# Performance work log

Measured on AMD Instinct MI355X. Metric: run time of the kernel, lower is better.

The kernel has to match this reference:

```python
import jax, jax.numpy as jnp
import numpy as np
import math

N_EMBD = 768
N_HEAD = 12
HEAD_DIM = N_EMBD // N_HEAD


def rope_cache(T, dim):
    # (T, dim//2, 2) with cos/sin of pos * inv_freq
    inv_freq = 1.0 / (10000.0 ** (2.0 * jnp.arange(dim // 2, dtype=jnp.float32) / dim))
    angles = jnp.arange(T, dtype=jnp.float32)[:, None] * inv_freq[None, :]
    return jnp.stack((jnp.cos(angles), jnp.sin(angles)), axis=-1)


def apply_rope(x, rope):
    # x: (B, H, T, D); rope: (T, D//2, 2)
    B, H, T, D = x.shape
    xp = x.reshape(B, H, T, D // 2, 2)
    x1, x2 = xp[..., 0], xp[..., 1]
    cos = rope[None, None, :, :, 0]
    sin = rope[None, None, :, :, 1]
    out = jnp.stack((x1 * cos - x2 * sin, x1 * sin + x2 * cos), axis=-1)
    return out.reshape(B, H, T, D)


def setup_inputs() -> dict:
    key = jax.random.key(0)
    ks = jax.random.split(key, 9)
    s = 0.02
    d = N_EMBD
    return {
        "x": jax.random.normal(ks[0], (2, 4096, d), dtype=jnp.float32),
        "Wq": jax.random.normal(ks[1], (d, d), dtype=jnp.float32) * s,
        "bq": jnp.zeros((d,), jnp.float32),
        "Wk": jax.random.normal(ks[2], (d, d), dtype=jnp.float32) * s,
        "bk": jnp.zeros((d,), jnp.float32),
        "Wv": jax.random.normal(ks[3], (d, d), dtype=jnp.float32) * s,
        "bv": jnp.zeros((d,), jnp.float32),
        "Wp": jax.random.normal(ks[4], (d, d), dtype=jnp.float32) * s,
        "bp": jnp.zeros((d,), jnp.float32),
    }


def reference(x, Wq, bq, Wk, bk, Wv, bv, Wp, bp):
    B, T, C = x.shape
    H, D = N_HEAD, HEAD_DIM

    def heads(W, b):
        return (x @ W.T + b).reshape(B, T, H, D).transpose(0, 2, 1, 3)

    q = heads(Wq, bq)
    k = heads(Wk, bk)
    v = heads(Wv, bv)
    rope = rope_cache(T, D)
    q = apply_rope(q, rope)
    k = apply_rope(k, rope)

    att = jnp.einsum('bhqd,bhkd->bhqk', q, k) * (1.0 / math.sqrt(D))
    causal = jnp.tril(jnp.ones((T, T), dtype=bool))
    att = jnp.where(causal[None, None], att, -jnp.inf)
    att = jax.nn.softmax(att, axis=-1)
    y = jnp.einsum('bhqk,bhkd->bhqd', att, v)
    y = y.transpose(0, 2, 1, 3).reshape(B, T, C)
    return y @ Wp.T + bp
```

## Files before the change

kernel.cpp:

```cpp
#include <hip/hip_runtime.h>
#include <hip/hip_bf16.h>

#define B_  2
#define T_  4096
#define C_  768
#define H_  12
#define D_  64
#define BT_ (B_*T_)

typedef __attribute__((ext_vector_type(8))) short short8;
typedef __attribute__((ext_vector_type(4))) short short4b;
typedef __attribute__((ext_vector_type(4))) float f32x4;

union U32x2 { unsigned u[2]; short4b s4; };

__device__ __forceinline__ ushort f2bf(float f) {
  union { __hip_bfloat16 b; ushort u; } cv; cv.b = __float2bfloat16(f); return cv.u;
}
__device__ __forceinline__ float bf2f(ushort u) {
  unsigned x = ((unsigned)u) << 16; float f; __builtin_memcpy(&f, &x, 4); return f;
}
__device__ __forceinline__ unsigned pack2(float a, float b) {
  return (unsigned)f2bf(a) | ((unsigned)f2bf(b) << 16);
}

__device__ __forceinline__ void gl16(const ushort* g, ushort* l) {
  typedef const __attribute__((address_space(1))) unsigned GU;
  typedef __attribute__((address_space(3))) unsigned LU;
  __builtin_amdgcn_global_load_lds((GU*)g, (LU*)l, 16, 0, 0);
}

__device__ __forceinline__ f32x4 mfma16(short4b a, short4b b, f32x4 c) {
#if __has_builtin(__builtin_amdgcn_mfma_f32_16x16x16bf16_1k)
  return __builtin_amdgcn_mfma_f32_16x16x16bf16_1k(a, b, c, 0, 0, 0);
#elif __has_builtin(__builtin_amdgcn_mfma_f32_16x16x16_bf16)
  return __builtin_amdgcn_mfma_f32_16x16x16_bf16(a, b, c, 0, 0, 0);
#else
  asm("v_mfma_f32_16x16x16_bf16 %0, %1, %2, %0" : "+v"(c) : "v"(a), "v"(b));
  return c;
#endif
}

__global__ void k_f32_to_bf16(const float* __restrict__ in, ushort* __restrict__ out, int n4) {
  int i = blockIdx.x * blockDim.x + threadIdx.x;
  if (i >= n4) return;
  const float4 v = ((const float4*)in)[i];
  ushort4 o;
  o.x = f2bf(v.x); o.y = f2bf(v.y); o.z = f2bf(v.z); o.w = f2bf(v.w);
  ((ushort4*)out)[i] = o;
}

__global__ void k_w_to_bf16(const float* __restrict__ w0, const float* __restrict__ w1,
                            const float* __restrict__ w2, const float* __restrict__ w3,
                            ushort* __restrict__ o0, ushort* __restrict__ o1,
                            ushort* __restrict__ o2, ushort* __restrict__ o3, int n4) {
  int i = blockIdx.x * blockDim.x + threadIdx.x;
  if (i >= n4) return;
  const int sel = blockIdx.y;
  const float* in = sel == 0 ? w0 : (sel == 1 ? w1 : (sel == 2 ? w2 : w3));
  ushort* out = sel == 0 ? o0 : (sel == 1 ? o1 : (sel == 2 ? o2 : o3));
  const float4 v = ((const float4*)in)[i];
  ushort4 o;
  o.x = f2bf(v.x); o.y = f2bf(v.y); o.z = f2bf(v.z); o.w = f2bf(v.w);
  ((ushort4*)out)[i] = o;
}

__global__ void k_rope_tab(float* __restrict__ ctab, float* __restrict__ stab) {
  int i = blockIdx.x * blockDim.x + threadIdx.x;
  int t = i >> 5, p = i & 31;
  float inv = 1.0f / powf(10000.0f, (2.0f * (float)p) / 64.0f);
  float a = (float)t * inv;
  ctab[i] = cosf(a); stab[i] = sinf(a);
}

__global__ __launch_bounds__(256) void k_qkv_gemm(
    const ushort* __restrict__ xb, const ushort* __restrict__ wq,
    const ushort* __restrict__ wk, const ushort* __restrict__ wv,
    const float* __restrict__ bq, const float* __restrict__ bk, const float* __restrict__ bv,
    const float* __restrict__ ctab, const float* __restrict__ stab,
    ushort* __restrict__ qo, ushort* __restrict__ ko, ushort* __restrict__ vo) {
  __shared__ __align__(16) ushort As[128 * 64];
  __shared__ __align__(16) ushort Bs[128 * 64];
  const int tid = threadIdx.x, l = tid & 63, w = tid >> 6;
  const int lr = l & 15, lg = l >> 4;
  const int m0 = blockIdx.x * 128;
  const int n0g = blockIdx.y * 128;
  const int proj = n0g / 768;
  const int n0 = n0g % 768;
  const ushort* wsrc = proj == 0 ? wq : (proj == 1 ? wk : wv);
  const int wr = (w >> 1) * 64, wc = (w & 1) * 64;

  f32x4 acc[4][4];
  #pragma unroll
  for (int a = 0; a < 4; ++a)
    #pragma unroll
    for (int b = 0; b < 4; ++b) acc[a][b] = (f32x4){0.f, 0.f, 0.f, 0.f};

  const int srow = w * 32 + (l >> 3);
  const int scg = ((l & 7) ^ (srow & 7)) * 8;

  for (int k0 = 0; k0 < 768; k0 += 64) {
    #pragma unroll
    for (int i = 0; i < 4; ++i) {
      const int row = srow + i * 8;
      gl16(xb + (size_t)(m0 + row) * 768 + k0 + scg, &As[(w * 32 + i * 8) * 64]);
      gl16(wsrc + (size_t)(n0 + row) * 768 + k0 + scg, &Bs[(w * 32 + i * 8) * 64]);
    }
    __syncthreads();
    #pragma unroll
    for (int kk = 0; kk < 2; ++kk) {
      short8 af[4], bf[4];
      #pragma unroll
      for (int mi = 0; mi < 4; ++mi) {
        const int row = wr + mi * 16 + lr;
        af[mi] = *(const short8*)&As[row * 64 + (((kk * 4 + lg) ^ (row & 7)) * 8)];
      }
      #pragma unroll
      for (int ni = 0; ni < 4; ++ni) {
        const int row = wc + ni * 16 + lr;
        bf[ni] = *(const short8*)&Bs[row * 64 + (((kk * 4 + lg) ^ (row & 7)) * 8)];
      }
      #pragma unroll
      for (int mi = 0; mi < 4; ++mi)
        #pragma unroll
        for (int ni = 0; ni < 4; ++ni)
          acc[mi][ni] = __builtin_amdgcn_mfma_f32_16x16x32_bf16(af[mi], bf[ni], acc[mi][ni], 0, 0, 0);
    }
    __syncthreads();
  }

  const float* bias = proj == 0 ? bq : (proj == 1 ? bk : bv);
  if (proj == 2) {
    #pragma unroll
    for (int mi = 0; mi < 4; ++mi) {
      #pragma unroll
      for (int ni = 0; ni < 4; ++ni) {
        int colc = n0 + wc + ni * 16 + lr;
        float bb = bias[colc];
        int h = colc >> 6, d = colc & 63;
        int row0 = m0 + wr + mi * 16 + lg * 4;
        int b = row0 >> 12, t0 = row0 & (T_ - 1);
        ushort4 pk;
        pk.x = f2bf(acc[mi][ni][0] + bb);
        pk.y = f2bf(acc[mi][ni][1] + bb);
        pk.z = f2bf(acc[mi][ni][2] + bb);
        pk.w = f2bf(acc[mi][ni][3] + bb);
        *(ushort4*)(vo + (((size_t)b * H_ + h) * 64 + d) * T_ + t0) = pk;
      }
    }
  } else {
    ushort* dst = proj == 0 ? qo : ko;
    const float qs = proj == 0 ? 0.18033688011112042f : 1.0f;
    #pragma unroll
    for (int mi = 0; mi < 4; ++mi) {
      #pragma unroll
      for (int ni = 0; ni < 4; ++ni) {
        int colc = n0 + wc + ni * 16 + lr;
        float bb = bias[colc];
        int h = colc >> 6, d = colc & 63;
        const int pidx = d >> 1;
        const bool evn = (d & 1) == 0;
        #pragma unroll
        for (int j = 0; j < 4; ++j) {
          int row = m0 + wr + mi * 16 + lg * 4 + j;
          int b = row >> 12, t = row & (T_ - 1);
          float val = acc[mi][ni][j] + bb;
          float prt = __shfl_xor(val, 1);
          float cc = ctab[(t << 5) + pidx];
          float ss = stab[(t << 5) + pidx];
          float ro = evn ? (val * cc - prt * ss) : (prt * ss + val * cc);
          dst[((((size_t)b * H_ + h) << 12) + t) * 64 + d] = f2bf(ro * qs);
        }
      }
    }
  }
}

__global__ __launch_bounds__(256) void k_proj_gemm(
    const ushort* __restrict__ yb, const ushort* __restrict__ wp,
    const float* __restrict__ bp, float* __restrict__ out) {
  __shared__ __align__(16) ushort As[64 * 64];
  __shared__ __align__(16) ushort Bs[128 * 64];
  const int tid = threadIdx.x, l = tid & 63, w = tid >> 6;
  const int lr = l & 15, lg = l >> 4;
  const int m0 = blockIdx.x * 64;
  const int n0 = blockIdx.y * 128;
  const int wc = w * 32;

  f32x4 acc[4][2];
  #pragma unroll
  for (int a = 0; a < 4; ++a)
    #pragma unroll
    for (int b = 0; b < 2; ++b) acc[a][b] = (f32x4){0.f, 0.f, 0.f, 0.f};

  const int srowA = w * 16 + (l >> 3);
  const int scgA = ((l & 7) ^ (srowA & 7)) * 8;
  const int srowB = w * 32 + (l >> 3);
  const int scgB = ((l & 7) ^ (srowB & 7)) * 8;

  for (int k0 = 0; k0 < 768; k0 += 64) {
    #pragma unroll
    for (int i = 0; i < 2; ++i) {
      const int row = srowA + i * 8;
      gl16(yb + (size_t)(m0 + row) * 768 + k0 + scgA, &As[(w * 16 + i * 8) * 64]);
    }
    #pragma unroll
    for (int i = 0; i < 4; ++i) {
      const int row = srowB + i * 8;
      gl16(wp + (size_t)(n0 + row) * 768 + k0 + scgB, &Bs[(w * 32 + i * 8) * 64]);
    }
    __syncthreads();
    #pragma unroll
    for (int kk = 0; kk < 2; ++kk) {
      short8 af[4], bf[2];
      #pragma unroll
      for (int mi = 0; mi < 4; ++mi) {
        const int row = mi * 16 + lr;
        af[mi] = *(const short8*)&As[row * 64 + (((kk * 4 + lg) ^ (row & 7)) * 8)];
      }
      #pragma unroll
      for (int ni = 0; ni < 2; ++ni) {
        const int row = wc + ni * 16 + lr;
        bf[ni] = *(const short8*)&Bs[row * 64 + (((kk * 4 + lg) ^ (row & 7)) * 8)];
      }
      #pragma unroll
      for (int mi = 0; mi < 4; ++mi)
        #pragma unroll
        for (int ni = 0; ni < 2; ++ni)
          acc[mi][ni] = __builtin_amdgcn_mfma_f32_16x16x32_bf16(af[mi], bf[ni], acc[mi][ni], 0, 0, 0);
    }
    __syncthreads();
  }

  #pragma unroll
  for (int mi = 0; mi < 4; ++mi)
    #pragma unroll
    for (int ni = 0; ni < 2; ++ni) {
      int col = n0 + wc + ni * 16 + lr;
      float bb = bp[col];
      #pragma unroll
      for (int j = 0; j < 4; ++j) {
        int row = m0 + mi * 16 + lg * 4 + j;
        out[(size_t)row * 768 + col] = acc[mi][ni][j] + bb;
      }
    }
}

__global__ __launch_bounds__(256) void k_attn(
    const ushort* __restrict__ q, const ushort* __restrict__ k,
    const ushort* __restrict__ vt, ushort* __restrict__ y) {
  __shared__ __align__(16) ushort Ks[2][64 * 64];
  __shared__ __align__(16) ushort Vs[2][64 * 64];
  const int tid = threadIdx.x, l = tid & 63, w = tid >> 6;
  const int lr = l & 15, lg = l >> 4;
  const int p = blockIdx.x & 31;
  const int bh = blockIdx.x >> 5;
  const size_t kpl = (size_t)bh * T_ * 64;
  const size_t vpl = (size_t)bh * 64 * T_;
  const int b = bh / H_, h = bh % H_;
  const short4b ones4 = { (short)0x3F80, (short)0x3F80, (short)0x3F80, (short)0x3F80 };

  #pragma unroll 1
  for (int ph = 0; ph < 2; ++ph) {
    const int t = ph == 0 ? p : 63 - p;
    const int nt = t + 1;
    const int qrow = t * 64 + w * 16 + lr;

    short8 qf[2];
    #pragma unroll
    for (int kk = 0; kk < 2; ++kk)
      qf[kk] = *(const short8*)(q + kpl + (size_t)qrow * 64 + kk * 32 + lg * 8);

    f32x4 o[4];
    f32x4 lsa = (f32x4){0.f, 0.f, 0.f, 0.f};
    float mx = 0.0f;
    #pragma unroll
    for (int c = 0; c < 4; ++c) o[c] = (f32x4){0.f, 0.f, 0.f, 0.f};

    __syncthreads();
    {
      #pragma unroll
      for (int i2 = 0; i2 < 2; ++i2) {
        const int r = w * 16 + i2 * 8 + (l >> 3);
        const int sl = (l & 7) ^ (r & 7);
        short8 s0 = *(const short8*)(k + kpl + (size_t)r * 64 + (l & 7) * 8);
        short8 v0 = *(const short8*)(vt + vpl + (size_t)r * T_ + (l & 7) * 8);
        *(short8*)&Ks[0][r * 64 + sl * 8] = s0;
        *(short8*)&Vs[0][r * 64 + sl * 8] = v0;
      }
    }

    int buf = 0;
    for (int kt = 0; kt < nt; ++kt) {
      __syncthreads();
      short8 sk[2], sv[2];
      const bool pre = (kt + 1 < nt);
      if (pre) {
        #pragma unroll
        for (int i2 = 0; i2 < 2; ++i2) {
          const int r = w * 16 + i2 * 8 + (l >> 3);
          sk[i2] = *(const short8*)(k + kpl + (size_t)((kt + 1) * 64 + r) * 64 + (l & 7) * 8);
          sv[i2] = *(const short8*)(vt + vpl + (size_t)r * T_ + (kt + 1) * 64 + (l & 7) * 8);
        }
      }

      const f32x4 zinit = (f32x4){-mx, -mx, -mx, -mx};
      f32x4 sT[4];
      __builtin_amdgcn_s_setprio(1);
      #pragma unroll
      for (int c = 0; c < 4; ++c) {
        short8 kf0 = *(const short8*)&Ks[buf][(c * 16 + lr) * 64 + ((lg) ^ (lr & 7)) * 8];
        short8 kf1 = *(const short8*)&Ks[buf][(c * 16 + lr) * 64 + ((4 + lg) ^ (lr & 7)) * 8];
        f32x4 z = zinit;
        z = __builtin_amdgcn_mfma_f32_16x16x32_bf16(kf0, qf[0], z, 0, 0, 0);
        z = __builtin_amdgcn_mfma_f32_16x16x32_bf16(kf1, qf[1], z, 0, 0, 0);
        sT[c] = z;
      }
      __builtin_amdgcn_s_setprio(0);

      if (kt == t) {
        #pragma unroll
        for (int c = 0; c < 4; ++c)
          #pragma unroll
          for (int jj = 0; jj < 4; ++jj)
            if (kt * 64 + c * 16 + lg * 4 + jj > qrow) sT[c][jj] = -1e30f;
      }

      const unsigned lbits = __builtin_bit_cast(unsigned, lsa[0]);
      if (lbits > 0x4B800000u) {
        const int e = (int)((lbits >> 23) & 0xFF) - 127;
        const float g = (float)e;
        const float corr = __builtin_bit_cast(float, (unsigned)((127 - e) << 23));
        mx += g;
        lsa *= corr;
        #pragma unroll
        for (int c = 0; c < 4; ++c) o[c] *= corr;
        #pragma unroll
        for (int c = 0; c < 4; ++c)
          #pragma unroll
          for (int jj = 0; jj < 4; ++jj) sT[c][jj] -= g;
      }
      U32x2 pb[4];
      #pragma unroll
      for (int c = 0; c < 4; ++c) {
        float p0 = exp2f(sT[c][0]);
        float p1 = exp2f(sT[c][1]);
        float p2 = exp2f(sT[c][2]);
        float p3 = exp2f(sT[c][3]);
        pb[c].u[0] = pack2(p0, p1); pb[c].u[1] = pack2(p2, p3);
      }

      __builtin_amdgcn_s_setprio(1);
      #pragma unroll
      for (int ks = 0; ks < 4; ++ks) {
        lsa = mfma16(ones4, pb[ks].s4, lsa);
        #pragma unroll
        for (int c = 0; c < 4; ++c) {
          const int row = c * 16 + lr;
          const int sl = (2 * ks + (lg >> 1)) ^ (row & 7);
          short4b va = *(const short4b*)&Vs[buf][row * 64 + sl * 8 + (lg & 1) * 4];
          o[c] = mfma16(va, pb[ks].s4, o[c]);
        }
      }
      __builtin_amdgcn_s_setprio(0);

      if (pre) {
        #pragma unroll
        for (int i2 = 0; i2 < 2; ++i2) {
          const int r = w * 16 + i2 * 8 + (l >> 3);
          const int sl = (l & 7) ^ (r & 7);
          *(short8*)&Ks[buf ^ 1][r * 64 + sl * 8] = sk[i2];
          *(short8*)&Vs[buf ^ 1][r * 64 + sl * 8] = sv[i2];
        }
      }
      buf ^= 1;
    }

    const float linv = 1.0f / lsa[0];
    const size_t base = ((size_t)b * T_ + qrow) * C_ + h * 64;
    #pragma unroll
    for (int c = 0; c < 4; ++c) {
      ushort4 pk;
      pk.x = f2bf(o[c][0] * linv);
      pk.y = f2bf(o[c][1] * linv);
      pk.z = f2bf(o[c][2] * linv);
      pk.w = f2bf(o[c][3] * linv);
      *(ushort4*)(y + base + c * 16 + lg * 4) = pk;
    }
  }
}

extern "C" void kernel_launch(void* const* d_in, const int* in_sizes, int n_in,
                              void* d_out, int out_size, void* d_ws, size_t ws_size,
                              hipStream_t stream) {
  const float* x  = (const float*)d_in[0];
  const float* Wq = (const float*)d_in[1];
  const float* bq = (const float*)d_in[2];
  const float* Wk = (const float*)d_in[3];
  const float* bk = (const float*)d_in[4];
  const float* Wv = (const float*)d_in[5];
  const float* bv = (const float*)d_in[6];
  const float* Wp = (const float*)d_in[7];
  const float* bp = (const float*)d_in[8];
  float* out = (float*)d_out;

  char* p = (char*)d_ws;
  auto alloc = [&](size_t bytes) { char* r = p; p += (bytes + 255) & ~255ULL; return r; };
  ushort* xb  = (ushort*)alloc((size_t)BT_ * C_ * 2);
  ushort* wqb = (ushort*)alloc((size_t)C_ * C_ * 2);
  ushort* wkb = (ushort*)alloc((size_t)C_ * C_ * 2);
  ushort* wvb = (ushort*)alloc((size_t)C_ * C_ * 2);
  ushort* wpb = (ushort*)alloc((size_t)C_ * C_ * 2);
  ushort* qb  = (ushort*)alloc((size_t)BT_ * C_ * 2);
  ushort* kb  = (ushort*)alloc((size_t)BT_ * C_ * 2);
  ushort* vtb = (ushort*)alloc((size_t)BT_ * C_ * 2);
  ushort* yb  = (ushort*)alloc((size_t)BT_ * C_ * 2);
  float* ctab = (float*)alloc((size_t)T_ * 32 * 4);
  float* stab = (float*)alloc((size_t)T_ * 32 * 4);

  k_f32_to_bf16<<<(BT_ * C_ / 4 + 255) / 256, 256, 0, stream>>>(x, xb, BT_ * C_ / 4);
  k_w_to_bf16<<<dim3((C_ * C_ / 4 + 255) / 256, 4), 256, 0, stream>>>(
      Wq, Wk, Wv, Wp, wqb, wkb, wvb, wpb, C_ * C_ / 4);
  k_rope_tab<<<T_ * 32 / 256, 256, 0, stream>>>(ctab, stab);

  k_qkv_gemm<<<dim3(BT_ / 128, 2304 / 128), 256, 0, stream>>>(
      xb, wqb, wkb, wvb, bq, bk, bv, ctab, stab, qb, kb, vtb);

  k_attn<<<dim3(768), 256, 0, stream>>>(qb, kb, vtb, yb);

  k_proj_gemm<<<dim3(BT_ / 64, C_ / 128), 256, 0, stream>>>(yb, wpb, bp, out);
}
```

Baseline: 204.0 us.

## Load K/V tiles directly into LDS with swizzled direct-to-LDS global loads

Replaces the register-staged K/V prefetch (global load into registers, then store to LDS after compute) with a gl16 helper that issues direct global-to-LDS loads. The XOR swizzle moves to the source address side so the LDS layout stays the same. The aim is to free VGPRs and drop the LDS store instructions and register round-trip, letting the prefetch overlap the MFMA work. Correctness depends on gl16 being defined earlier and on the barriers and waits covering the asynchronous LDS writes.

```diff
diff --git a/kernel.cpp b/kernel.cpp
--- a/kernel.cpp
+++ b/kernel.cpp
@@ -260,6 +260,8 @@
   const int b = bh / H_, h = bh % H_;
   const short4b ones4 = { (short)0x3F80, (short)0x3F80, (short)0x3F80, (short)0x3F80 };
 
+  const int sc8 = ((l & 7) ^ ((l >> 3) & 7)) * 8;
+
   #pragma unroll 1
   for (int ph = 0; ph < 2; ++ph) {
     const int t = ph == 0 ? p : 63 - p;
@@ -277,31 +279,29 @@
     #pragma unroll
     for (int c = 0; c < 4; ++c) o[c] = (f32x4){0.f, 0.f, 0.f, 0.f};
 
+    const ushort* kg0 = k + kpl + (size_t)(w * 16 + (l >> 3)) * 64 + sc8;
+    const ushort* kg1 = kg0 + 8 * 64;
+    const ushort* vg0 = vt + vpl + (size_t)(w * 16 + (l >> 3)) * T_ + sc8;
+    const ushort* vg1 = vg0 + 8 * T_;
+
     __syncthreads();
-    {
-      #pragma unroll
-      for (int i2 = 0; i2 < 2; ++i2) {
-        const int r = w * 16 + i2 * 8 + (l >> 3);
-        const int sl = (l & 7) ^ (r & 7);
-        short8 s0 = *(const short8*)(k + kpl + (size_t)r * 64 + (l & 7) * 8);
-        short8 v0 = *(const short8*)(vt + vpl + (size_t)r * T_ + (l & 7) * 8);
-        *(short8*)&Ks[0][r * 64 + sl * 8] = s0;
-        *(short8*)&Vs[0][r * 64 + sl * 8] = v0;
-      }
-    }
+    gl16(kg0, &Ks[0][(w * 16) * 64]);
+    gl16(kg1, &Ks[0][(w * 16 + 8) * 64]);
+    gl16(vg0, &Vs[0][(w * 16) * 64]);
+    gl16(vg1, &Vs[0][(w * 16 + 8) * 64]);
+    kg0 += 4096; kg1 += 4096; vg0 += 64; vg1 += 64;
 
     int buf = 0;
     for (int kt = 0; kt < nt; ++kt) {
       __syncthreads();
-      short8 sk[2], sv[2];
-      const bool pre = (kt + 1 < nt);
-      if (pre) {
-        #pragma unroll
-        for (int i2 = 0; i2 < 2; ++i2) {
-          const int r = w * 16 + i2 * 8 + (l >> 3);
-          sk[i2] = *(const short8*)(k + kpl + (size_t)((kt + 1) * 64 + r) * 64 + (l & 7) * 8);
-          sv[i2] = *(const short8*)(vt + vpl + (size_t)r * T_ + (kt + 1) * 64 + (l & 7) * 8);
-        }
+      if (kt + 1 < nt) {
+        ushort* kd = &Ks[buf ^ 1][0];
+        ushort* vd = &Vs[buf ^ 1][0];
+        gl16(kg0, kd + (w * 16) * 64);
+        gl16(kg1, kd + (w * 16 + 8) * 64);
+        gl16(vg0, vd + (w * 16) * 64);
+        gl16(vg1, vd + (w * 16 + 8) * 64);
+        kg0 += 4096; kg1 += 4096; vg0 += 64; vg1 += 64;
       }
 
       const f32x4 zinit = (f32x4){-mx, -mx, -mx, -mx};
@@ -364,15 +364,6 @@
       }
       __builtin_amdgcn_s_setprio(0);
 
-      if (pre) {
-        #pragma unroll
-        for (int i2 = 0; i2 < 2; ++i2) {
-          const int r = w * 16 + i2 * 8 + (l >> 3);
-          const int sl = (l & 7) ^ (r & 7);
-          *(short8*)&Ks[buf ^ 1][r * 64 + sl * 8] = sk[i2];
-          *(short8*)&Vs[buf ^ 1][r * 64 + sl * 8] = sv[i2];
-        }
-      }
       buf ^= 1;
     }
 
```

New measurement: 219.5 us. 1.08x slower.
